# Optimization experiments

Hardware: AMD Instinct MI355X
Metric: run time of the kernel (lower is better)

Reference implementation:

```python
import jax, jax.numpy as jnp
import numpy as np

EMB = 300      # node embedding dim (GNNGraph default)
NL = 5         # num GNN layers
G = 4096       # number of graphs in batch
ATOM_F, ATOM_V = 9, 128   # OGB-style atom encoder: 9 categorical feats
BOND_F, BOND_V = 3, 8     # OGB-style bond encoder: 3 categorical feats
BN_EPS = 1e-5


def _bn(x, g, b, m, v):
    # BatchNorm1d in eval mode (running stats)
    return (x - m) * jax.lax.rsqrt(v + BN_EPS) * g + b


def _gnn(x, edge_index, edge_attr, batch,
         atom_emb, bond_emb, vn_emb,
         gin_eps, gin_W1, gin_b1, gin_bn1_g, gin_bn1_b, gin_bn1_m, gin_bn1_v,
         gin_W2, gin_b2, bn_g, bn_b, bn_m, bn_v,
         vn_W1, vn_b1, vn_bn1_g, vn_bn1_b, vn_bn1_m, vn_bn1_v,
         vn_W2, vn_b2, vn_bn2_g, vn_bn2_b, vn_bn2_m, vn_bn2_v):
    N = x.shape[0]
    # AtomEncoder / BondEncoder: sum of per-feature embedding lookups
    h = atom_emb[jnp.arange(ATOM_F)[None, :], x].sum(axis=1)          # [N, EMB]
    e = bond_emb[jnp.arange(BOND_F)[None, :], edge_attr].sum(axis=1)  # [E, EMB]
    row, col = edge_index[0], edge_index[1]
    # virtual node embedding, one per graph
    vn = jnp.broadcast_to(vn_emb[0], (G, EMB))
    for l in range(NL):
        h = h + vn[batch]                                   # broadcast virtual node
        # GINConv: message = relu(x_j + edge_emb), aggr = scatter-add at target
        msg = jax.nn.relu(h[row] + e)                       # [E, EMB]
        agg = jax.ops.segment_sum(msg, col, num_segments=N) # [N, EMB]
        t = (1.0 + gin_eps[l]) * h + agg
        t = jnp.dot(t, gin_W1[l]) + gin_b1[l]               # [N, 2*EMB]
        t = jax.nn.relu(_bn(t, gin_bn1_g[l], gin_bn1_b[l], gin_bn1_m[l], gin_bn1_v[l]))
        t = jnp.dot(t, gin_W2[l]) + gin_b2[l]               # [N, EMB]
        hn = _bn(t, bn_g[l], bn_b[l], bn_m[l], bn_v[l])     # outer BatchNorm
        if l < NL - 1:
            hn = jax.nn.relu(hn)                            # (dropout inactive in eval)
            # virtual node update: global_add_pool(h_list[layer]) + vn -> MLP
            pooled = jax.ops.segment_sum(h, batch, num_segments=G) + vn
            u = jnp.dot(pooled, vn_W1[l]) + vn_b1[l]
            u = jax.nn.relu(_bn(u, vn_bn1_g[l], vn_bn1_b[l], vn_bn1_m[l], vn_bn1_v[l]))
            u = jnp.dot(u, vn_W2[l]) + vn_b2[l]
            vn = jax.nn.relu(_bn(u, vn_bn2_g[l], vn_bn2_b[l], vn_bn2_m[l], vn_bn2_v[l]))
        h = hn
    # global_mean_pool over graphs
    counts = jax.ops.segment_sum(jnp.ones((N,), h.dtype), batch, num_segments=G)
    return jax.ops.segment_sum(h, batch, num_segments=G) / jnp.maximum(counts, 1.0)[:, None]


def setup_inputs() -> dict:
    key = jax.random.key(0)
    ks = iter(jax.random.split(key, 64))
    N, E = 100000, 250000
    d = {}
    d['x'] = jax.random.randint(next(ks), (N, ATOM_F), 0, ATOM_V, dtype=jnp.int32)
    d['edge_index'] = jax.random.randint(next(ks), (2, E), 0, N, dtype=jnp.int32)
    d['edge_attr'] = jax.random.randint(next(ks), (E, BOND_F), 0, BOND_V, dtype=jnp.int32)
    d['batch'] = jnp.sort(jax.random.randint(next(ks), (N,), 0, G, dtype=jnp.int32))
    s = 0.05
    d['atom_emb'] = jax.random.normal(next(ks), (ATOM_F, ATOM_V, EMB), jnp.float32) * s
    d['bond_emb'] = jax.random.normal(next(ks), (BOND_F, BOND_V, EMB), jnp.float32) * s
    d['vn_emb'] = jax.random.normal(next(ks), (1, EMB), jnp.float32) * s
    d['gin_eps'] = jax.random.normal(next(ks), (NL,), jnp.float32) * 0.01
    d['gin_W1'] = jax.random.normal(next(ks), (NL, EMB, 2 * EMB), jnp.float32) * s
    d['gin_b1'] = jax.random.normal(next(ks), (NL, 2 * EMB), jnp.float32) * s
    d['gin_bn1_g'] = 1.0 + jax.random.normal(next(ks), (NL, 2 * EMB), jnp.float32) * s
    d['gin_bn1_b'] = jax.random.normal(next(ks), (NL, 2 * EMB), jnp.float32) * s
    d['gin_bn1_m'] = jax.random.normal(next(ks), (NL, 2 * EMB), jnp.float32) * s
    d['gin_bn1_v'] = jax.random.uniform(next(ks), (NL, 2 * EMB), jnp.float32) + 0.5
    d['gin_W2'] = jax.random.normal(next(ks), (NL, 2 * EMB, EMB), jnp.float32) * s
    d['gin_b2'] = jax.random.normal(next(ks), (NL, EMB), jnp.float32) * s
    d['bn_g'] = 1.0 + jax.random.normal(next(ks), (NL, EMB), jnp.float32) * s
    d['bn_b'] = jax.random.normal(next(ks), (NL, EMB), jnp.float32) * s
    d['bn_m'] = jax.random.normal(next(ks), (NL, EMB), jnp.float32) * s
    d['bn_v'] = jax.random.uniform(next(ks), (NL, EMB), jnp.float32) + 0.5
    V = NL - 1
    d['vn_W1'] = jax.random.normal(next(ks), (V, EMB, 2 * EMB), jnp.float32) * s
    d['vn_b1'] = jax.random.normal(next(ks), (V, 2 * EMB), jnp.float32) * s
    d['vn_bn1_g'] = 1.0 + jax.random.normal(next(ks), (V, 2 * EMB), jnp.float32) * s
    d['vn_bn1_b'] = jax.random.normal(next(ks), (V, 2 * EMB), jnp.float32) * s
    d['vn_bn1_m'] = jax.random.normal(next(ks), (V, 2 * EMB), jnp.float32) * s
    d['vn_bn1_v'] = jax.random.uniform(next(ks), (V, 2 * EMB), jnp.float32) + 0.5
    d['vn_W2'] = jax.random.normal(next(ks), (V, 2 * EMB, EMB), jnp.float32) * s
    d['vn_b2'] = jax.random.normal(next(ks), (V, EMB), jnp.float32) * s
    d['vn_bn2_g'] = 1.0 + jax.random.normal(next(ks), (V, EMB), jnp.float32) * s
    d['vn_bn2_b'] = jax.random.normal(next(ks), (V, EMB), jnp.float32) * s
    d['vn_bn2_m'] = jax.random.normal(next(ks), (V, EMB), jnp.float32) * s
    d['vn_bn2_v'] = jax.random.uniform(next(ks), (V, EMB), jnp.float32) + 0.5
    return d


def reference(x, edge_index, edge_attr, batch,
              atom_emb, bond_emb, vn_emb,
              gin_eps, gin_W1, gin_b1, gin_bn1_g, gin_bn1_b, gin_bn1_m, gin_bn1_v,
              gin_W2, gin_b2, bn_g, bn_b, bn_m, bn_v,
              vn_W1, vn_b1, vn_bn1_g, vn_bn1_b, vn_bn1_m, vn_bn1_v,
              vn_W2, vn_b2, vn_bn2_g, vn_bn2_b, vn_bn2_m, vn_bn2_v):
    return _gnn(x, edge_index, edge_attr, batch,
                atom_emb, bond_emb, vn_emb,
                gin_eps, gin_W1, gin_b1, gin_bn1_g, gin_bn1_b, gin_bn1_m, gin_bn1_v,
                gin_W2, gin_b2, bn_g, bn_b, bn_m, bn_v,
                vn_W1, vn_b1, vn_bn1_g, vn_bn1_b, vn_bn1_m, vn_bn1_v,
                vn_W2, vn_b2, vn_bn2_g, vn_bn2_b, vn_bn2_m, vn_bn2_v)
```

## Files before the change

kernel.cpp:

```cpp
#include <hip/hip_runtime.h>
#include <hip/hip_bf16.h>

#define EMBD 300
#define GG   4096
#define NLAY 5
#define KP1  320
#define KP2  640
#define NP1  640
#define NP2  384
#define WPER (NP1*KP1 + NP2*KP2)

typedef unsigned short ushort_t;
typedef short short8 __attribute__((ext_vector_type(8)));
typedef short short4v __attribute__((ext_vector_type(4)));
typedef float f32x4 __attribute__((ext_vector_type(4)));

static inline int cdiv(int a, int b) { return (a + b - 1) / b; }


__device__ inline void dma16(const ushort_t* g, ushort_t* l) {
    __builtin_amdgcn_global_load_lds(
        (const __attribute__((address_space(1))) unsigned int*)g,
        (__attribute__((address_space(3))) unsigned int*)l, 16, 0, 0);
}

__device__ inline ushort_t bf16_of(float v) {
    union { __hip_bfloat16 b; ushort_t u; } c;
    c.b = __float2bfloat16(v);
    return c.u;
}

__device__ inline float bf2f(ushort_t u) {
    union { unsigned int i; float f; } c;
    c.i = ((unsigned int)u) << 16;
    return c.f;
}


__global__ void atom_encode_bf(const int* __restrict__ x, const float* __restrict__ aemb,
                               ushort_t* __restrict__ h, int N) {
    int i = blockIdx.x * blockDim.x + threadIdx.x;
    int total = N * 75;
    if (i >= total) return;
    int n = i / 75, d4 = i - n * 75;
    const int* xr = x + n * 9;
    float4 s = make_float4(0.f, 0.f, 0.f, 0.f);
    const float4* a4 = (const float4*)aemb;
#pragma unroll
    for (int f = 0; f < 9; ++f) {
        float4 v = a4[(size_t)((f << 7) + xr[f]) * 75 + d4];
        s.x += v.x; s.y += v.y; s.z += v.z; s.w += v.w;
    }
    short4v o;
    o[0] = (short)bf16_of(s.x); o[1] = (short)bf16_of(s.y);
    o[2] = (short)bf16_of(s.z); o[3] = (short)bf16_of(s.w);
    *(short4v*)(h + (size_t)n * KP1 + d4 * 4) = o;
}

__global__ void init_vn4(const float* __restrict__ vn_emb, float* __restrict__ vn) {
    int i = blockIdx.x * blockDim.x + threadIdx.x;
    if (i >= GG * 75) return;
    ((float4*)vn)[i] = ((const float4*)vn_emb)[i % 75];
}

__global__ void find_starts(const int* __restrict__ batch, int* __restrict__ starts, int N) {
    int g = blockIdx.x * blockDim.x + threadIdx.x;
    if (g > GG) return;
    int lo = 0, hi = N;
    while (lo < hi) {
        int mid = (lo + hi) >> 1;
        if (batch[mid] < g) lo = mid + 1; else hi = mid;
    }
    starts[g] = lo;
}

__global__ void bond_combo(const float* __restrict__ bemb, float* __restrict__ ebsum) {
    int i = blockIdx.x * blockDim.x + threadIdx.x;
    if (i >= 512 * EMBD) return;
    int c = i / EMBD, d = i - c * EMBD;
    int a0 = c >> 6, a1 = (c >> 3) & 7, a2 = c & 7;
    ebsum[i] = bemb[a0 * EMBD + d] + bemb[(8 + a1) * EMBD + d] + bemb[(16 + a2) * EMBD + d];
}

__global__ void conv_all(const float* __restrict__ gW1, const float* __restrict__ gW2,
                         const float* __restrict__ vW1, const float* __restrict__ vW2,
                         ushort_t* __restrict__ wh) {
    int i = blockIdx.x * blockDim.x + threadIdx.x;
    int total = WPER * 9;
    if (i >= total) return;
    int mlp = i / WPER, r = i - mlp * WPER;
    const float *W1, *W2;
    if (mlp < NLAY) {
        W1 = gW1 + (size_t)mlp * EMBD * 2 * EMBD;
        W2 = gW2 + (size_t)mlp * 2 * EMBD * EMBD;
    } else {
        int l = mlp - NLAY;
        W1 = vW1 + (size_t)l * EMBD * 2 * EMBD;
        W2 = vW2 + (size_t)l * 2 * EMBD * EMBD;
    }
    float v;
    if (r < NP1 * KP1) {
        int n = r / KP1, k = r - n * KP1;
        v = (n < 2 * EMBD && k < EMBD) ? W1[(size_t)k * (2 * EMBD) + n] : 0.f;
    } else {
        int r2 = r - NP1 * KP1;
        int n = r2 / KP2, k = r2 - n * KP2;
        v = (n < EMBD && k < 2 * EMBD) ? W2[(size_t)k * EMBD + n] : 0.f;
    }
    wh[i] = bf16_of(v);
}


__global__ void ecount(const int* __restrict__ ei, int* __restrict__ cnt, int E) {
    int e = blockIdx.x * blockDim.x + threadIdx.x;
    if (e >= E) return;
    atomicAdd(&cnt[ei[E + e]], 1);
}

__global__ void scan_part(const int* __restrict__ cnt, int* __restrict__ bsum, int N) {
    __shared__ int sh[256];
    int b = blockIdx.x, t = threadIdx.x;
    int base = b * 1024;
    int s = 0;
    for (int j = t; j < 1024; j += 256) {
        int idx = base + j;
        if (idx < N) s += cnt[idx];
    }
    sh[t] = s;
    __syncthreads();
    for (int d = 128; d > 0; d >>= 1) {
        if (t < d) sh[t] += sh[t + d];
        __syncthreads();
    }
    if (t == 0) bsum[b] = sh[0];
}

__global__ void scan_top(int* __restrict__ bsum, int nb) {
    __shared__ int sh[1024];
    int t = threadIdx.x;
    int v = (t < nb) ? bsum[t] : 0;
    sh[t] = v;
    __syncthreads();
    for (int d = 1; d < 1024; d <<= 1) {
        int u = (t >= d) ? sh[t - d] : 0;
        __syncthreads();
        sh[t] += u;
        __syncthreads();
    }
    if (t < nb) bsum[t] = sh[t] - v;
}

__global__ void scan_final(const int* __restrict__ cnt, const int* __restrict__ bsum,
                           int* __restrict__ estart, int* __restrict__ cursor, int N, int E) {
    __shared__ int sh[256];
    int b = blockIdx.x, t = threadIdx.x;
    int base = b * 1024 + t * 4;
    int c[4];
    int s = 0;
#pragma unroll
    for (int j = 0; j < 4; ++j) {
        int idx = base + j;
        c[j] = (idx < N) ? cnt[idx] : 0;
        s += c[j];
    }
    sh[t] = s;
    __syncthreads();
    for (int d = 1; d < 256; d <<= 1) {
        int u = (t >= d) ? sh[t - d] : 0;
        __syncthreads();
        sh[t] += u;
        __syncthreads();
    }
    int run = sh[t] - s + bsum[b];
#pragma unroll
    for (int j = 0; j < 4; ++j) {
        int idx = base + j;
        if (idx < N) { estart[idx] = run; cursor[idx] = run; run += c[j]; }
    }
    if (b == 0 && t == 0) estart[N] = E;
}

__global__ void escatter(const int* __restrict__ ei, const int* __restrict__ ea,
                         int* __restrict__ cursor, int2* __restrict__ epack, int E) {
    int e = blockIdx.x * blockDim.x + threadIdx.x;
    if (e >= E) return;
    int c = ei[E + e];
    int p = atomicAdd(&cursor[c], 1);
    epack[p] = make_int2(ei[e], (ea[3 * e] << 6) | (ea[3 * e + 1] << 3) | ea[3 * e + 2]);
}


__global__ void pool_prep(ushort_t* __restrict__ h, const float* __restrict__ vn,
                          const int* __restrict__ starts, ushort_t* __restrict__ vnaB) {
    int g = blockIdx.x;
    int t = threadIdx.x;
    if (t >= EMBD) return;
    float vng = vn[(size_t)g * EMBD + t];
    int s0 = starts[g], s1 = starts[g + 1];
    float s = 0.f;
    for (int n = s0; n < s1; ++n) {
        size_t idx = (size_t)n * KP1 + t;
        float v = bf2f(h[idx]) + vng;
        h[idx] = bf16_of(v);
        s += v;
    }
    vnaB[(size_t)g * KP1 + t] = bf16_of(s + vng);
}

__global__ void prep_vn(ushort_t* __restrict__ h, const float* __restrict__ vn,
                        const int* __restrict__ batch, int N) {
    int i = blockIdx.x * blockDim.x + threadIdx.x;
    int total = N * 75;
    if (i >= total) return;
    int n = i / 75, d4 = i - n * 75;
    float4 vv = ((const float4*)vn)[(size_t)batch[n] * 75 + d4];
    short4v hv = *(short4v*)(h + (size_t)n * KP1 + d4 * 4);
    short4v o;
    o[0] = (short)bf16_of(bf2f((ushort_t)hv[0]) + vv.x);
    o[1] = (short)bf16_of(bf2f((ushort_t)hv[1]) + vv.y);
    o[2] = (short)bf16_of(bf2f((ushort_t)hv[2]) + vv.z);
    o[3] = (short)bf16_of(bf2f((ushort_t)hv[3]) + vv.w);
    *(short4v*)(h + (size_t)n * KP1 + d4 * 4) = o;
}

__global__ void pool_mean(const ushort_t* __restrict__ h, const int* __restrict__ starts,
                          float* __restrict__ out) {
    int g = blockIdx.x;
    int t = threadIdx.x;
    if (t >= EMBD) return;
    int s0 = starts[g], s1 = starts[g + 1];
    float s = 0.f;
    for (int n = s0; n < s1; ++n) s += bf2f(h[(size_t)n * KP1 + t]);
    float cnt = (float)(s1 - s0);
    out[(size_t)g * EMBD + t] = s / fmaxf(cnt, 1.0f);
}

#define NPB 4

__global__ void aggregate(const ushort_t* __restrict__ h, const float* __restrict__ ebsum,
                          const int* __restrict__ estart, const int2* __restrict__ epack,
                          const float* __restrict__ epsp,
                          ushort_t* __restrict__ aggB, int N) {
    int n = blockIdx.x * NPB + threadIdx.x / 80;
    int slot = threadIdx.x % 80;
    if (n >= N) return;
    float4 acc = make_float4(0.f, 0.f, 0.f, 0.f);
    if (slot < 75) {
        const float4* b4 = (const float4*)ebsum;
        float ce = 1.0f + *epsp;
        short4v hv = *(const short4v*)(h + (size_t)n * KP1 + slot * 4);
        acc.x = ce * bf2f((ushort_t)hv[0]);
        acc.y = ce * bf2f((ushort_t)hv[1]);
        acc.z = ce * bf2f((ushort_t)hv[2]);
        acc.w = ce * bf2f((ushort_t)hv[3]);
        int p0 = estart[n], p1 = estart[n + 1];
        for (int p = p0; p < p1; ++p) {
            int2 ep = epack[p];
            short4v xv = *(const short4v*)(h + (size_t)ep.x * KP1 + slot * 4);
            float4 ev = b4[(size_t)ep.y * 75 + slot];
            acc.x += fmaxf(bf2f((ushort_t)xv[0]) + ev.x, 0.f);
            acc.y += fmaxf(bf2f((ushort_t)xv[1]) + ev.y, 0.f);
            acc.z += fmaxf(bf2f((ushort_t)xv[2]) + ev.z, 0.f);
            acc.w += fmaxf(bf2f((ushort_t)xv[3]) + ev.w, 0.f);
        }
    }
    short4v bv4;
    bv4[0] = (short)bf16_of(acc.x);
    bv4[1] = (short)bf16_of(acc.y);
    bv4[2] = (short)bf16_of(acc.z);
    bv4[3] = (short)bf16_of(acc.w);
    *(short4v*)(aggB + (size_t)n * KP1 + slot * 4) = bv4;
}

#define BMg 128
#define BNg 128

__global__ __launch_bounds__(256) void gemm_as(
    const ushort_t* __restrict__ A, int KP,
    const ushort_t* __restrict__ B,
    const float* __restrict__ bias, const float* __restrict__ gg,
    const float* __restrict__ bb, const float* __restrict__ bm,
    const float* __restrict__ bv,
    int Mc, int NnReal, int relu, int nb, int mb,
    float* __restrict__ outF, int ldF,
    ushort_t* __restrict__ outB, int ldP)
{
    __shared__ ushort_t sA[2][BMg * 32];
    __shared__ ushort_t sB[2][BNg * 32];

    int id = blockIdx.x;
    int hi = id / (8 * nb);
    int rem = id - hi * 8 * nb;
    int xcd = rem & 7;
    int nblk = rem >> 3;
    int mblk = hi * 8 + xcd;
    if (mblk >= mb) return;

    const int tid = threadIdx.x;
    const int lane = tid & 63;
    const int w = tid >> 6;
    const int m0 = mblk * BMg;
    const int n0 = nblk * BNg;
    const int wm = (w & 1) * 64;
    const int wn = (w >> 1) * 64;

    const ushort_t* gA[2];
    const ushort_t* gB[2];
    int lbase[2];
#pragma unroll
    for (int i = 0; i < 2; ++i) {
        int s = tid + 256 * i;
        int m = s >> 2, qp = s & 3;
        int q = (qp - (m >> 1)) & 3;
        int msrc = (m0 + m < Mc) ? (m0 + m) : (Mc - 1);
        gA[i] = A + (size_t)msrc * KP + 8 * q;
        gB[i] = B + (size_t)(n0 + m) * KP + 8 * q;
        lbase[i] = (w * 64 + 256 * i) * 8;
    }

    f32x4 acc[4][4];
#pragma unroll
    for (int a = 0; a < 4; ++a)
#pragma unroll
        for (int b = 0; b < 4; ++b) acc[a][b] = (f32x4)(0.f);

    const int q = lane >> 4;
    const int c16 = lane & 15;
    const int kt = KP >> 5;

#pragma unroll
    for (int i = 0; i < 2; ++i) {
        dma16(gA[i], sA[0] + lbase[i]); gA[i] += 32;
        dma16(gB[i], sB[0] + lbase[i]); gB[i] += 32;
    }
    __syncthreads();

    for (int t = 0; t < kt; ++t) {
        int cur = t & 1, nxt = cur ^ 1;
        if (t + 1 < kt) {
#pragma unroll
            for (int i = 0; i < 2; ++i) {
                dma16(gA[i], sA[nxt] + lbase[i]); gA[i] += 32;
                dma16(gB[i], sB[nxt] + lbase[i]); gB[i] += 32;
            }
        }
        short8 av[4], bhv[4];
#pragma unroll
        for (int tt = 0; tt < 4; ++tt) {
            int m = wm + tt * 16 + c16;
            int q2 = (q + (m >> 1)) & 3;
            av[tt] = *(const short8*)(sA[cur] + m * 32 + q2 * 8);
        }
#pragma unroll
        for (int uu = 0; uu < 4; ++uu) {
            int n = wn + uu * 16 + c16;
            int q2 = (q + (n >> 1)) & 3;
            bhv[uu] = *(const short8*)(sB[cur] + n * 32 + q2 * 8);
        }
#pragma unroll
        for (int tt = 0; tt < 4; ++tt)
#pragma unroll
            for (int uu = 0; uu < 4; ++uu)
                acc[tt][uu] = __builtin_amdgcn_mfma_f32_16x16x32_bf16(av[tt], bhv[uu], acc[tt][uu], 0, 0, 0);
        __syncthreads();
    }

#pragma unroll
    for (int uu = 0; uu < 4; ++uu) {
        int gn = n0 + wn + uu * 16 + c16;
        float sc = 0.f, sh = 0.f;
        if (gn < NnReal) {
            sc = gg[gn] * rsqrtf(bv[gn] + 1e-5f);
            sh = bb[gn] + (bias[gn] - bm[gn]) * sc;
        }
#pragma unroll
        for (int tt = 0; tt < 4; ++tt) {
            int rbase = m0 + wm + tt * 16 + q * 4;
#pragma unroll
            for (int r = 0; r < 4; ++r) {
                int gm = rbase + r;
                if (gm >= Mc) continue;
                float y = acc[tt][uu][r] * sc + sh;
                if (relu) y = fmaxf(y, 0.f);
                if (outF) {
                    if (gn < NnReal) outF[(size_t)gm * ldF + gn] = y;
                } else {
                    if (gn < ldP) outB[(size_t)gm * ldP + gn] = bf16_of(y);
                }
            }
        }
    }
}


struct MlpP {
    const float *b1, *g1, *be1, *m1, *v1;
    const float *b2, *g2, *be2, *m2, *v2;
};

static void run_mlp(hipStream_t stream, const ushort_t* inB, int M,
                    const ushort_t* wh, int mlp,
                    ushort_t* tB, int CH,
                    const MlpP& W, ushort_t* outB, int relu2) {
    const ushort_t* w1 = wh + (size_t)mlp * WPER;
    const ushort_t* w2 = w1 + NP1 * KP1;
    for (int c0 = 0; c0 < M; c0 += CH) {
        int Mc = (M - c0 < CH) ? (M - c0) : CH;
        int mb = cdiv(Mc, BMg);
        int mbp = cdiv(mb, 8) * 8;
        {
            int nb = NP1 / BNg;
            gemm_as<<<nb * mbp, 256, 0, stream>>>(
                inB + (size_t)c0 * KP1, KP1, w1,
                W.b1, W.g1, W.be1, W.m1, W.v1,
                Mc, 2 * EMBD, 1, nb, mb,
                nullptr, 0, tB, KP2);
        }
        {
            int nb = NP2 / BNg;
            gemm_as<<<nb * mbp, 256, 0, stream>>>(
                tB, KP2, w2,
                W.b2, W.g2, W.be2, W.m2, W.v2,
                Mc, EMBD, relu2, nb, mb,
                nullptr, 0, outB + (size_t)c0 * KP1, KP1);
        }
    }
}


extern "C" void kernel_launch(void* const* d_in, const int* in_sizes, int n_in,
                              void* d_out, int out_size, void* d_ws, size_t ws_size,
                              hipStream_t stream) {
    const int*   x        = (const int*)d_in[0];
    const int*   ei       = (const int*)d_in[1];
    const int*   ea       = (const int*)d_in[2];
    const int*   batch    = (const int*)d_in[3];
    const float* atom_emb = (const float*)d_in[4];
    const float* bond_emb = (const float*)d_in[5];
    const float* vn_emb   = (const float*)d_in[6];
    const float* gin_eps  = (const float*)d_in[7];
    const float* gin_W1   = (const float*)d_in[8];
    const float* gin_b1   = (const float*)d_in[9];
    const float* gin_bn1g = (const float*)d_in[10];
    const float* gin_bn1b = (const float*)d_in[11];
    const float* gin_bn1m = (const float*)d_in[12];
    const float* gin_bn1v = (const float*)d_in[13];
    const float* gin_W2   = (const float*)d_in[14];
    const float* gin_b2   = (const float*)d_in[15];
    const float* bn_g     = (const float*)d_in[16];
    const float* bn_b     = (const float*)d_in[17];
    const float* bn_m     = (const float*)d_in[18];
    const float* bn_v     = (const float*)d_in[19];
    const float* vn_W1    = (const float*)d_in[20];
    const float* vn_b1    = (const float*)d_in[21];
    const float* vn_bn1g  = (const float*)d_in[22];
    const float* vn_bn1b  = (const float*)d_in[23];
    const float* vn_bn1m  = (const float*)d_in[24];
    const float* vn_bn1v  = (const float*)d_in[25];
    const float* vn_W2    = (const float*)d_in[26];
    const float* vn_b2    = (const float*)d_in[27];
    const float* vn_bn2g  = (const float*)d_in[28];
    const float* vn_bn2b  = (const float*)d_in[29];
    const float* vn_bn2m  = (const float*)d_in[30];
    const float* vn_bn2v  = (const float*)d_in[31];

    const int N = in_sizes[3];
    const int E = in_sizes[1] / 2;
    const int NB = cdiv(N, 1024);

    char* base = (char*)d_ws;
    size_t off = 0;
    ushort_t* hbuf = (ushort_t*)(base + off); off += (size_t)N * KP1 * 2;
    ushort_t* aggB = (ushort_t*)(base + off); off += (size_t)N * KP1 * 2;
    float* vnbuf   = (float*)(base + off);    off += (size_t)GG * EMBD * 4;
    int*   starts  = (int*)(base + off);      off += 4104 * 4;
    int*   cnt     = (int*)(base + off);      off += (size_t)N * 4;
    int*   cursor  = (int*)(base + off);      off += (size_t)N * 4;
    int*   estart  = (int*)(base + off);      off += ((size_t)N + 8) * 4;
    int*   bsum    = (int*)(base + off);      off += 1032 * 4;
    int2*  epack   = (int2*)(base + off);     off += (size_t)E * 8;
    float* ebsum   = (float*)(base + off);    off += (size_t)512 * EMBD * 4;
    ushort_t* whA  = (ushort_t*)(base + off); off += (size_t)9 * WPER * 2;
    ushort_t* vnaB = (ushort_t*)(base + off); off += (size_t)GG * KP1 * 2;
    off = (off + 255) & ~(size_t)255;

    size_t avail = (ws_size > off) ? ws_size - off : 0;
    int CH = (int)(avail / (KP2 * 2));
    CH &= ~255;
    if (CH > N) CH = (N + 255) & ~255;
    else if (CH >= (N + 1) / 2) CH = (((N + 1) / 2) + 255) & ~255;
    if (CH < 2048) CH = 2048;
    ushort_t* tB = (ushort_t*)(base + off);

    const int BLK = 256;
    int ne4 = N * 75;

    find_starts<<<cdiv(GG + 1, BLK), BLK, 0, stream>>>(batch, starts, N);
    atom_encode_bf<<<cdiv(ne4, BLK), BLK, 0, stream>>>(x, atom_emb, hbuf, N);
    init_vn4<<<cdiv(GG * 75, BLK), BLK, 0, stream>>>(vn_emb, vnbuf);
    bond_combo<<<cdiv(512 * EMBD, BLK), BLK, 0, stream>>>(bond_emb, ebsum);
    conv_all<<<cdiv(9 * WPER, BLK), BLK, 0, stream>>>(gin_W1, gin_W2, vn_W1, vn_W2, whA);
    hipMemsetAsync(cnt, 0, (size_t)N * 4, stream);
    hipMemsetAsync(vnaB, 0, (size_t)GG * KP1 * 2, stream);
    ecount<<<cdiv(E, BLK), BLK, 0, stream>>>(ei, cnt, E);
    scan_part<<<NB, 256, 0, stream>>>(cnt, bsum, N);
    scan_top<<<1, 1024, 0, stream>>>(bsum, NB);
    scan_final<<<NB, 256, 0, stream>>>(cnt, bsum, estart, cursor, N, E);
    escatter<<<cdiv(E, BLK), BLK, 0, stream>>>(ei, ea, cursor, epack, E);

    for (int l = 0; l < NLAY; ++l) {
        int last = (l == NLAY - 1);

        if (!last)
            pool_prep<<<GG, 320, 0, stream>>>(hbuf, vnbuf, starts, vnaB);
        else
            prep_vn<<<cdiv(ne4, BLK), BLK, 0, stream>>>(hbuf, vnbuf, batch, N);

        aggregate<<<cdiv(N, NPB), NPB * 80, 0, stream>>>(
            hbuf, ebsum, estart, epack, gin_eps + l, aggB, N);

        MlpP Wn = { gin_b1 + (size_t)l * 2 * EMBD,
                    gin_bn1g + (size_t)l * 2 * EMBD, gin_bn1b + (size_t)l * 2 * EMBD,
                    gin_bn1m + (size_t)l * 2 * EMBD, gin_bn1v + (size_t)l * 2 * EMBD,
                    gin_b2 + (size_t)l * EMBD,
                    bn_g + (size_t)l * EMBD, bn_b + (size_t)l * EMBD,
                    bn_m + (size_t)l * EMBD, bn_v + (size_t)l * EMBD };
        run_mlp(stream, aggB, N, whA, l, tB, CH, Wn, hbuf, last ? 0 : 1);

        if (!last) {
            MlpP Wv = { vn_b1 + (size_t)l * 2 * EMBD,
                        vn_bn1g + (size_t)l * 2 * EMBD, vn_bn1b + (size_t)l * 2 * EMBD,
                        vn_bn1m + (size_t)l * 2 * EMBD, vn_bn1v + (size_t)l * 2 * EMBD,
                        vn_b2 + (size_t)l * EMBD,
                        vn_bn2g + (size_t)l * EMBD, vn_bn2b + (size_t)l * EMBD,
                        vn_bn2m + (size_t)l * EMBD, vn_bn2v + (size_t)l * EMBD };
            const ushort_t* w1 = whA + (size_t)(NLAY + l) * WPER;
            const ushort_t* w2 = w1 + NP1 * KP1;
            int mb = cdiv(GG, BMg), mbp = cdiv(mb, 8) * 8;
            gemm_as<<<(NP1 / BNg) * mbp, 256, 0, stream>>>(
                vnaB, KP1, w1,
                vn_b1 + (size_t)l * 2 * EMBD, vn_bn1g + (size_t)l * 2 * EMBD,
                vn_bn1b + (size_t)l * 2 * EMBD, vn_bn1m + (size_t)l * 2 * EMBD,
                vn_bn1v + (size_t)l * 2 * EMBD,
                GG, 2 * EMBD, 1, NP1 / BNg, mb,
                nullptr, 0, tB, KP2);
            gemm_as<<<(NP2 / BNg) * mbp, 256, 0, stream>>>(
                tB, KP2, w2,
                vn_b2 + (size_t)l * EMBD, vn_bn2g + (size_t)l * EMBD,
                vn_bn2b + (size_t)l * EMBD, vn_bn2m + (size_t)l * EMBD,
                vn_bn2v + (size_t)l * EMBD,
                GG, EMBD, 1, NP2 / BNg, mb,
                vnbuf, EMBD, nullptr, 0);
        }
    }

    pool_mean<<<GG, 320, 0, stream>>>(hbuf, starts, (float*)d_out);
}
```

Baseline: 1.934 ms.

## Pack edges into one int, vectorize pooling, unroll aggregation, narrow hidden stride

Edge records are packed into a single 32-bit int (source index shifted left by 9, bond combo in the low bits), which halves edge-list traffic. The aggregate loop is unrolled by two so more gathers are in flight. pool_prep and pool_mean now use float4/short4 vector accesses and handle four graphs per block. The MLP hidden buffer stride drops from 640 to 608, cutting the second GEMM's K loop by one tile, and the count array is reused as the scatter cursor. Risks: the narrower hidden stride is only safe if the first GEMM writes no padded columns beyond 608, and the packed int limits the node count to about 2^22.

```diff
diff --git a/kernel.cpp b/kernel.cpp
--- a/kernel.cpp
+++ b/kernel.cpp
@@ -6,6 +6,7 @@
 #define NLAY 5
 #define KP1  320
 #define KP2  640
+#define KT2  608
 #define NP1  640
 #define NP2  384
 #define WPER (NP1*KP1 + NP2*KP2)
@@ -150,7 +151,7 @@
     if (t < nb) bsum[t] = sh[t] - v;
 }
 
-__global__ void scan_final(const int* __restrict__ cnt, const int* __restrict__ bsum,
+__global__ void scan_final(int* __restrict__ cnt, const int* __restrict__ bsum,
                            int* __restrict__ estart, int* __restrict__ cursor, int N, int E) {
     __shared__ int sh[256];
     int b = blockIdx.x, t = threadIdx.x;
@@ -181,30 +182,40 @@
 }
 
 __global__ void escatter(const int* __restrict__ ei, const int* __restrict__ ea,
-                         int* __restrict__ cursor, int2* __restrict__ epack, int E) {
+                         int* __restrict__ cursor, int* __restrict__ epack, int E) {
     int e = blockIdx.x * blockDim.x + threadIdx.x;
     if (e >= E) return;
     int c = ei[E + e];
     int p = atomicAdd(&cursor[c], 1);
-    epack[p] = make_int2(ei[e], (ea[3 * e] << 6) | (ea[3 * e + 1] << 3) | ea[3 * e + 2]);
+    epack[p] = (ei[e] << 9) | (ea[3 * e] << 6) | (ea[3 * e + 1] << 3) | ea[3 * e + 2];
 }
 
 
 __global__ void pool_prep(ushort_t* __restrict__ h, const float* __restrict__ vn,
                           const int* __restrict__ starts, ushort_t* __restrict__ vnaB) {
-    int g = blockIdx.x;
-    int t = threadIdx.x;
-    if (t >= EMBD) return;
-    float vng = vn[(size_t)g * EMBD + t];
+    int g = blockIdx.x * 4 + threadIdx.x / 80;
+    int slot = threadIdx.x % 80;
+    if (g >= GG || slot >= 75) return;
+    float4 vng = ((const float4*)vn)[(size_t)g * 75 + slot];
     int s0 = starts[g], s1 = starts[g + 1];
-    float s = 0.f;
+    float4 s = make_float4(0.f, 0.f, 0.f, 0.f);
     for (int n = s0; n < s1; ++n) {
-        size_t idx = (size_t)n * KP1 + t;
-        float v = bf2f(h[idx]) + vng;
-        h[idx] = bf16_of(v);
-        s += v;
-    }
-    vnaB[(size_t)g * KP1 + t] = bf16_of(s + vng);
+        short4v* hp = (short4v*)(h + (size_t)n * KP1 + slot * 4);
+        short4v hv = *hp;
+        float v0 = bf2f((ushort_t)hv[0]) + vng.x;
+        float v1 = bf2f((ushort_t)hv[1]) + vng.y;
+        float v2 = bf2f((ushort_t)hv[2]) + vng.z;
+        float v3 = bf2f((ushort_t)hv[3]) + vng.w;
+        short4v o;
+        o[0] = (short)bf16_of(v0); o[1] = (short)bf16_of(v1);
+        o[2] = (short)bf16_of(v2); o[3] = (short)bf16_of(v3);
+        *hp = o;
+        s.x += v0; s.y += v1; s.z += v2; s.w += v3;
+    }
+    short4v o;
+    o[0] = (short)bf16_of(s.x + vng.x); o[1] = (short)bf16_of(s.y + vng.y);
+    o[2] = (short)bf16_of(s.z + vng.z); o[3] = (short)bf16_of(s.w + vng.w);
+    *(short4v*)(vnaB + (size_t)g * KP1 + slot * 4) = o;
 }
 
 __global__ void prep_vn(ushort_t* __restrict__ h, const float* __restrict__ vn,
@@ -225,20 +236,27 @@
 
 __global__ void pool_mean(const ushort_t* __restrict__ h, const int* __restrict__ starts,
                           float* __restrict__ out) {
-    int g = blockIdx.x;
-    int t = threadIdx.x;
-    if (t >= EMBD) return;
+    int g = blockIdx.x * 4 + threadIdx.x / 80;
+    int slot = threadIdx.x % 80;
+    if (g >= GG || slot >= 75) return;
     int s0 = starts[g], s1 = starts[g + 1];
-    float s = 0.f;
-    for (int n = s0; n < s1; ++n) s += bf2f(h[(size_t)n * KP1 + t]);
-    float cnt = (float)(s1 - s0);
-    out[(size_t)g * EMBD + t] = s / fmaxf(cnt, 1.0f);
+    float4 s = make_float4(0.f, 0.f, 0.f, 0.f);
+    for (int n = s0; n < s1; ++n) {
+        short4v hv = *(const short4v*)(h + (size_t)n * KP1 + slot * 4);
+        s.x += bf2f((ushort_t)hv[0]);
+        s.y += bf2f((ushort_t)hv[1]);
+        s.z += bf2f((ushort_t)hv[2]);
+        s.w += bf2f((ushort_t)hv[3]);
+    }
+    float inv = 1.0f / fmaxf((float)(s1 - s0), 1.0f);
+    float4 o = make_float4(s.x * inv, s.y * inv, s.z * inv, s.w * inv);
+    ((float4*)out)[(size_t)g * 75 + slot] = o;
 }
 
 #define NPB 4
 
 __global__ void aggregate(const ushort_t* __restrict__ h, const float* __restrict__ ebsum,
-                          const int* __restrict__ estart, const int2* __restrict__ epack,
+                          const int* __restrict__ estart, const int* __restrict__ epack,
                           const float* __restrict__ epsp,
                           ushort_t* __restrict__ aggB, int N) {
     int n = blockIdx.x * NPB + threadIdx.x / 80;
@@ -254,14 +272,26 @@
         acc.z = ce * bf2f((ushort_t)hv[2]);
         acc.w = ce * bf2f((ushort_t)hv[3]);
         int p0 = estart[n], p1 = estart[n + 1];
-        for (int p = p0; p < p1; ++p) {
-            int2 ep = epack[p];
-            short4v xv = *(const short4v*)(h + (size_t)ep.x * KP1 + slot * 4);
-            float4 ev = b4[(size_t)ep.y * 75 + slot];
-            acc.x += fmaxf(bf2f((ushort_t)xv[0]) + ev.x, 0.f);
-            acc.y += fmaxf(bf2f((ushort_t)xv[1]) + ev.y, 0.f);
-            acc.z += fmaxf(bf2f((ushort_t)xv[2]) + ev.z, 0.f);
-            acc.w += fmaxf(bf2f((ushort_t)xv[3]) + ev.w, 0.f);
+        int p = p0;
+        for (; p + 2 <= p1; p += 2) {
+            int e0 = epack[p], e1 = epack[p + 1];
+            short4v xv0 = *(const short4v*)(h + (size_t)(e0 >> 9) * KP1 + slot * 4);
+            short4v xv1 = *(const short4v*)(h + (size_t)(e1 >> 9) * KP1 + slot * 4);
+            float4 ev0 = b4[(size_t)(e0 & 511) * 75 + slot];
+            float4 ev1 = b4[(size_t)(e1 & 511) * 75 + slot];
+            acc.x += fmaxf(bf2f((ushort_t)xv0[0]) + ev0.x, 0.f) + fmaxf(bf2f((ushort_t)xv1[0]) + ev1.x, 0.f);
+            acc.y += fmaxf(bf2f((ushort_t)xv0[1]) + ev0.y, 0.f) + fmaxf(bf2f((ushort_t)xv1[1]) + ev1.y, 0.f);
+            acc.z += fmaxf(bf2f((ushort_t)xv0[2]) + ev0.z, 0.f) + fmaxf(bf2f((ushort_t)xv1[2]) + ev1.z, 0.f);
+            acc.w += fmaxf(bf2f((ushort_t)xv0[3]) + ev0.w, 0.f) + fmaxf(bf2f((ushort_t)xv1[3]) + ev1.w, 0.f);
+        }
+        if (p < p1) {
+            int e0 = epack[p];
+            short4v xv0 = *(const short4v*)(h + (size_t)(e0 >> 9) * KP1 + slot * 4);
+            float4 ev0 = b4[(size_t)(e0 & 511) * 75 + slot];
+            acc.x += fmaxf(bf2f((ushort_t)xv0[0]) + ev0.x, 0.f);
+            acc.y += fmaxf(bf2f((ushort_t)xv0[1]) + ev0.y, 0.f);
+            acc.z += fmaxf(bf2f((ushort_t)xv0[2]) + ev0.z, 0.f);
+            acc.w += fmaxf(bf2f((ushort_t)xv0[3]) + ev0.w, 0.f);
         }
     }
     short4v bv4;
@@ -276,8 +306,8 @@
 #define BNg 128
 
 __global__ __launch_bounds__(256) void gemm_as(
-    const ushort_t* __restrict__ A, int KP,
-    const ushort_t* __restrict__ B,
+    const ushort_t* __restrict__ A, int KPA,
+    const ushort_t* __restrict__ B, int KPB,
     const float* __restrict__ bias, const float* __restrict__ gg,
     const float* __restrict__ bb, const float* __restrict__ bm,
     const float* __restrict__ bv,
@@ -313,8 +343,8 @@
         int m = s >> 2, qp = s & 3;
         int q = (qp - (m >> 1)) & 3;
         int msrc = (m0 + m < Mc) ? (m0 + m) : (Mc - 1);
-        gA[i] = A + (size_t)msrc * KP + 8 * q;
-        gB[i] = B + (size_t)(n0 + m) * KP + 8 * q;
+        gA[i] = A + (size_t)msrc * KPA + 8 * q;
+        gB[i] = B + (size_t)(n0 + m) * KPB + 8 * q;
         lbase[i] = (w * 64 + 256 * i) * 8;
     }
 
@@ -326,7 +356,7 @@
 
     const int q = lane >> 4;
     const int c16 = lane & 15;
-    const int kt = KP >> 5;
+    const int kt = KPA >> 5;
 
 #pragma unroll
     for (int i = 0; i < 2; ++i) {
@@ -411,15 +441,15 @@
         {
             int nb = NP1 / BNg;
             gemm_as<<<nb * mbp, 256, 0, stream>>>(
-                inB + (size_t)c0 * KP1, KP1, w1,
+                inB + (size_t)c0 * KP1, KP1, w1, KP1,
                 W.b1, W.g1, W.be1, W.m1, W.v1,
                 Mc, 2 * EMBD, 1, nb, mb,
-                nullptr, 0, tB, KP2);
+                nullptr, 0, tB, KT2);
         }
         {
             int nb = NP2 / BNg;
             gemm_as<<<nb * mbp, 256, 0, stream>>>(
-                tB, KP2, w2,
+                tB, KT2, w2, KP2,
                 W.b2, W.g2, W.be2, W.m2, W.v2,
                 Mc, EMBD, relu2, nb, mb,
                 nullptr, 0, outB + (size_t)c0 * KP1, KP1);
@@ -475,19 +505,18 @@
     float* vnbuf   = (float*)(base + off);    off += (size_t)GG * EMBD * 4;
     int*   starts  = (int*)(base + off);      off += 4104 * 4;
     int*   cnt     = (int*)(base + off);      off += (size_t)N * 4;
-    int*   cursor  = (int*)(base + off);      off += (size_t)N * 4;
     int*   estart  = (int*)(base + off);      off += ((size_t)N + 8) * 4;
     int*   bsum    = (int*)(base + off);      off += 1032 * 4;
-    int2*  epack   = (int2*)(base + off);     off += (size_t)E * 8;
+    int*   epack   = (int*)(base + off);      off += (size_t)E * 4;
     float* ebsum   = (float*)(base + off);    off += (size_t)512 * EMBD * 4;
     ushort_t* whA  = (ushort_t*)(base + off); off += (size_t)9 * WPER * 2;
     ushort_t* vnaB = (ushort_t*)(base + off); off += (size_t)GG * KP1 * 2;
     off = (off + 255) & ~(size_t)255;
 
     size_t avail = (ws_size > off) ? ws_size - off : 0;
-    int CH = (int)(avail / (KP2 * 2));
+    int CH = (int)(avail / (KT2 * 2));
     CH &= ~255;
-    if (CH > N) CH = (N + 255) & ~255;
+    if (CH >= N) CH = (N + 255) & ~255;
     else if (CH >= (N + 1) / 2) CH = (((N + 1) / 2) + 255) & ~255;
     if (CH < 2048) CH = 2048;
     ushort_t* tB = (ushort_t*)(base + off);
@@ -505,14 +534,14 @@
     ecount<<<cdiv(E, BLK), BLK, 0, stream>>>(ei, cnt, E);
     scan_part<<<NB, 256, 0, stream>>>(cnt, bsum, N);
     scan_top<<<1, 1024, 0, stream>>>(bsum, NB);
-    scan_final<<<NB, 256, 0, stream>>>(cnt, bsum, estart, cursor, N, E);
-    escatter<<<cdiv(E, BLK), BLK, 0, stream>>>(ei, ea, cursor, epack, E);
+    scan_final<<<NB, 256, 0, stream>>>(cnt, bsum, estart, cnt , N, E);
+    escatter<<<cdiv(E, BLK), BLK, 0, stream>>>(ei, ea, cnt , epack, E);
 
     for (int l = 0; l < NLAY; ++l) {
         int last = (l == NLAY - 1);
 
         if (!last)
-            pool_prep<<<GG, 320, 0, stream>>>(hbuf, vnbuf, starts, vnaB);
+            pool_prep<<<GG / 4, 320, 0, stream>>>(hbuf, vnbuf, starts, vnaB);
         else
             prep_vn<<<cdiv(ne4, BLK), BLK, 0, stream>>>(hbuf, vnbuf, batch, N);
 
@@ -528,24 +557,18 @@
         run_mlp(stream, aggB, N, whA, l, tB, CH, Wn, hbuf, last ? 0 : 1);
 
         if (!last) {
-            MlpP Wv = { vn_b1 + (size_t)l * 2 * EMBD,
-                        vn_bn1g + (size_t)l * 2 * EMBD, vn_bn1b + (size_t)l * 2 * EMBD,
-                        vn_bn1m + (size_t)l * 2 * EMBD, vn_bn1v + (size_t)l * 2 * EMBD,
-                        vn_b2 + (size_t)l * EMBD,
-                        vn_bn2g + (size_t)l * EMBD, vn_bn2b + (size_t)l * EMBD,
-                        vn_bn2m + (size_t)l * EMBD, vn_bn2v + (size_t)l * EMBD };
             const ushort_t* w1 = whA + (size_t)(NLAY + l) * WPER;
             const ushort_t* w2 = w1 + NP1 * KP1;
             int mb = cdiv(GG, BMg), mbp = cdiv(mb, 8) * 8;
             gemm_as<<<(NP1 / BNg) * mbp, 256, 0, stream>>>(
-                vnaB, KP1, w1,
+                vnaB, KP1, w1, KP1,
                 vn_b1 + (size_t)l * 2 * EMBD, vn_bn1g + (size_t)l * 2 * EMBD,
                 vn_bn1b + (size_t)l * 2 * EMBD, vn_bn1m + (size_t)l * 2 * EMBD,
                 vn_bn1v + (size_t)l * 2 * EMBD,
                 GG, 2 * EMBD, 1, NP1 / BNg, mb,
-                nullptr, 0, tB, KP2);
+                nullptr, 0, tB, KT2);
             gemm_as<<<(NP2 / BNg) * mbp, 256, 0, stream>>>(
-                tB, KP2, w2,
+                tB, KT2, w2, KP2,
                 vn_b2 + (size_t)l * EMBD, vn_bn2g + (size_t)l * EMBD,
                 vn_bn2b + (size_t)l * EMBD, vn_bn2m + (size_t)l * EMBD,
                 vn_bn2v + (size_t)l * EMBD,
@@ -554,5 +577,5 @@
         }
     }
 
-    pool_mean<<<GG, 320, 0, stream>>>(hbuf, starts, (float*)d_out);
-}
+    pool_mean<<<GG / 4, 320, 0, stream>>>(hbuf, starts, (float*)d_out);
+}
```

After: 1.749 ms. 9.6% less time.
